# Performance work log

Measured on AMD Instinct MI355X. Metric: run time of the kernel, lower is better.

Reference implementation:

```python
import jax, jax.numpy as jnp
import numpy as np

INPUT_DIM = 10
SIG_DEPTH = 3
HIDDEN = 64
D_AUG = INPUT_DIM + 1  # time augmentation
LOGSIG_DIM = min(sum(D_AUG ** k // max(1, k) for k in range(1, SIG_DEPTH + 1)), 512)  # = 512
B, N = 1024, 256


def _compute_logsigs(features):
    """Vectorized computation of the per-step prefix-path signature features.

    For prefix length k+1 the torch code time-augments with linspace(0,1,k+1),
    i.e. dt = 1/k, which makes the time-related signature terms k-dependent.
    All terms reduce to cumulative sums over t, computed once for all k.
    Returns (B, N, LOGSIG_DIM); row k=0 is zeros (torch uses zeros at k=0).
    """
    Bsz, n, D = features.shape
    d = D + 1  # augmented dim (time first)
    dtype = features.dtype
    x0 = features[:, :1, :]
    inc = features[:, 1:, :] - features[:, :-1, :]          # (B, n-1, D) feature increments
    rel = features - x0                                      # x_t - x_0, (B, n, D)
    t_idx = jnp.arange(n - 1, dtype=dtype)
    # A[k-1] = sum_{t<k} t * dx_t   (time-row of level-2 term, before dt scaling)
    A = jnp.cumsum(t_idx[None, :, None] * inc, axis=1)       # (B, n-1, D)
    # Bc[k-1] = sum_{t=0}^{k-1} (x_t - x_0)   (time-column, before dt scaling)
    Bc = jnp.cumsum(rel[:, :-1, :], axis=1)                  # (B, n-1, D)
    # C[k-1] = sum_{t<k} (x_t - x_0) outer dx_t  (feature-feature level-2 block)
    C = jnp.cumsum(rel[:, :-1, :, None] * inc[:, :, None, :], axis=1)  # (B, n-1, D, D)
    ks = jnp.arange(1, n, dtype=dtype)                       # k = 1..n-1
    inv_k = 1.0 / ks
    tt = 0.5 * (ks - 1) * inv_k                              # sum t*dt^2 = (k-1)/(2k)
    # level-1: [T=1, x_k - x_0]
    sig1 = jnp.concatenate([jnp.ones((Bsz, n - 1, 1), dtype), rel[:, 1:, :]], axis=-1)  # (B, n-1, d)
    # level-2 matrix, augmented order [time, features]
    sig2 = jnp.zeros((Bsz, n - 1, d, d), dtype)
    sig2 = sig2.at[:, :, 0, 0].set(tt[None, :])
    sig2 = sig2.at[:, :, 0, 1:].set(inv_k[None, :, None] * A)
    sig2 = sig2.at[:, :, 1:, 0].set(inv_k[None, :, None] * Bc)
    sig2 = sig2.at[:, :, 1:, 1:].set(C)
    sig2f = sig2.reshape(Bsz, n - 1, d * d)
    # level-3 (torch: flatten(sig1 outer sig2_flat), truncated); only build needed rows
    sig3_len = LOGSIG_DIM - d - d * d                        # 512 - 11 - 121 = 380
    rows = (sig3_len + d * d - 1) // (d * d)                 # 4 rows of sig1 suffice
    sig3 = (sig1[..., :rows, None] * sig2f[..., None, :]).reshape(Bsz, n - 1, rows * d * d)[..., :sig3_len]
    logsig = jnp.concatenate([sig1, sig2f, sig3], axis=-1)[..., :LOGSIG_DIM]  # (B, n-1, 512)
    return jnp.concatenate([jnp.zeros((Bsz, 1, LOGSIG_DIM), dtype), logsig], axis=1)


def setup_inputs() -> dict:
    key = jax.random.key(0)
    k0, k1, k2, k3 = jax.random.split(key, 4)
    features = jax.random.normal(k0, (B, N, INPUT_DIM), jnp.float32)
    in_dim = LOGSIG_DIM + INPUT_DIM + 1  # 523
    W1 = jax.random.normal(k1, (in_dim, HIDDEN), jnp.float32) / np.sqrt(in_dim)
    b1 = jnp.zeros((HIDDEN,), jnp.float32)
    W2 = jax.random.normal(k2, (HIDDEN, HIDDEN), jnp.float32) / np.sqrt(HIDDEN)
    b2 = jnp.zeros((HIDDEN,), jnp.float32)
    W3 = jax.random.normal(k3, (HIDDEN, 1), jnp.float32) / np.sqrt(HIDDEN)
    b3 = jnp.zeros((1,), jnp.float32)
    return {"features": features, "W1": W1, "b1": b1, "W2": W2, "b2": b2, "W3": W3, "b3": b3}


def reference(features, W1, b1, W2, b2, W3, b3):
    logsigs = _compute_logsigs(features)  # (B, N, LOGSIG_DIM)
    Bsz = features.shape[0]

    def step(prev_delta, inputs):
        ls, ft = inputs  # (B, L), (B, D)
        x = jnp.concatenate([ls, ft, prev_delta], axis=-1)
        h = jax.nn.relu(x @ W1 + b1)
        h = jax.nn.relu(h @ W2 + b2)
        delta = h @ W3 + b3  # (B, 1)
        return delta, delta[:, 0]

    ls_t = jnp.swapaxes(logsigs, 0, 1)   # (N, B, L)
    ft_t = jnp.swapaxes(features, 0, 1)  # (N, B, D)
    _, deltas = jax.lax.scan(step, jnp.zeros((Bsz, 1), features.dtype), (ls_t, ft_t))
    return jnp.swapaxes(deltas, 0, 1)    # (B, N)
```

## Files before the change

### kernel.cpp

```cpp
#include <hip/hip_runtime.h>

#define NB 1024
#define NT 256
#define IND 10
#define HID 64

#define KSTEPS 14
#define XS 456
#define WMF_HALVES (KSTEPS * 4 * 64 * 8)

typedef short bf16x8 __attribute__((ext_vector_type(8)));
typedef float f32x4 __attribute__((ext_vector_type(4)));

__device__ __forceinline__ int qmap(int kk) {
    if (kk < 10) return 1 + kk;
    if (kk < 20) return 11 * (kk - 10 + 1);
    int i = (kk - 20) / 10, c = (kk - 20) % 10;
    return 11 * (i + 1) + 1 + c;
}

__device__ __forceinline__ unsigned bf16rne(float x) {
    unsigned u = __float_as_uint(x);
    return (u + 0x7fffu + ((u >> 16) & 1u)) >> 16;
}
__device__ __forceinline__ unsigned pk2(float a, float b) {
    return bf16rne(a) | (bf16rne(b) << 16);
}

__device__ float wm_value(int kk, int j, const float* __restrict__ W1,
                          const float* __restrict__ b1) {
    if (kk < 384) {
        int sec = kk >> 7;
        int rem = kk & 127;
        int w = rem >> 5, i = rem & 31;
        if (i >= 30) return 0.f;
        int q = qmap(30 * w + i);
        if (sec == 0) return W1[(11 + q) * 64 + j] + W1[(132 + q) * 64 + j];
        if (sec == 1) return W1[(253 + q) * 64 + j];
        return W1[(374 + q) * 64 + j];
    }
    if (kk < 400) {
        int i = kk - 384;
        if (i < 10) return W1[(496 + i) * 64 + j];
        if (i == 10) return W1[506 * 64 + j];
        return W1[(507 + (i - 11)) * 64 + j];
    }
    if (kk < 410) return W1[(1 + (kk - 400)) * 64 + j];
    if (kk < 420) return W1[(512 + (kk - 410)) * 64 + j];
    if (kk == 420) return W1[11 * 64 + j] + W1[132 * 64 + j];
    if (kk == 421) return W1[253 * 64 + j];
    if (kk == 422) return W1[374 * 64 + j];
    if (kk == 423) return W1[495 * 64 + j];
    if (kk == 424) return W1[0 * 64 + j];
    if (kk == 425) return b1[j];
    return 0.f;
}

__global__ void pack_mfma_kernel(const float* __restrict__ W1,
                                 const float* __restrict__ b1,
                                 unsigned short* __restrict__ Wmf) {
    int idx = blockIdx.x * 256 + threadIdx.x;
    if (idx >= WMF_HALVES) return;
    int half = idx & 7;
    int lane = (idx >> 3) & 63;
    int rec = idx >> 9;
    int s = rec >> 2, jb = rec & 3;
    int kk = 32 * s + (lane >> 4) * 8 + half;
    int j = 16 * jb + (lane & 15);
    Wmf[idx] = (unsigned short)bf16rne(wm_value(kk, j, W1, b1));
}

__global__ __launch_bounds__(256, 1) void presig9_kernel(
    const float* __restrict__ features, const unsigned short* __restrict__ Wmf,
    float* __restrict__ pre1) {
    const int b = blockIdx.x;
    const int tid = threadIdx.x;
    const int l = tid & 63;
    const int wu = tid >> 6;

    __shared__ __align__(16) float sF[NT * IND];
    __shared__ __align__(16) unsigned short sX[64 * XS];
    __shared__ float sBase[128];

    {
        const float4* src = (const float4*)(features + b * (NT * IND));
        float4* dst = (float4*)sF;
        for (int e = tid; e < NT * IND / 4; e += 256) dst[e] = src[e];
    }
    float f0[IND];
#pragma unroll
    for (int c = 0; c < IND; ++c) f0[c] = features[b * (NT * IND) + c];

    if (tid < 128) sBase[tid] = 0.f;
    __syncthreads();

    for (int tile = 0; tile < 4; ++tile) {
        const int t0 = tile * 64;

        const int r = t0 + l;
        float rf = (float)r;
        float fr[IND], rel[IND], inc[IND];
#pragma unroll
        for (int c = 0; c < IND; ++c) fr[c] = sF[r * IND + c];
#pragma unroll
        for (int c = 0; c < IND; ++c) rel[c] = fr[c] - f0[c];
        {
            bool last = (r >= NT - 1);
#pragma unroll
            for (int c = 0; c < IND; ++c)
                inc[c] = last ? 0.f : (sF[(r + 1) * IND + c] - fr[c]);
        }
        float p[30], own[30];
        if (wu == 0) {
#pragma unroll
            for (int c = 0; c < 10; ++c) p[c] = rf * inc[c];
#pragma unroll
            for (int i = 0; i < 10; ++i) p[10 + i] = rel[i];
#pragma unroll
            for (int c = 0; c < 10; ++c) p[20 + c] = rel[0] * inc[c];
        } else {
            const int i0 = 3 * wu - 2;
#pragma unroll
            for (int q = 0; q < 30; ++q) {
                int i = i0 + q / 10, c = q % 10;
                p[q] = rel[i] * inc[c];
            }
        }
#pragma unroll
        for (int i = 0; i < 30; ++i) own[i] = p[i];
#pragma unroll
        for (int dsh = 0; dsh < 6; ++dsh) {
            const int d = 1 << dsh;
            bool ok = (l >= d);
#pragma unroll
            for (int i = 0; i < 30; ++i) {
                float v = __shfl_up(p[i], d, 64);
                if (ok) p[i] += v;
            }
        }
        float inv_r = (r > 0) ? 1.f / rf : 0.f;
        float v[30];
#pragma unroll
        for (int i = 0; i < 30; ++i) {
            float x = sBase[wu * 32 + i] + p[i] - own[i];
            if (wu == 0 && i < 20) x *= inv_r;
            v[i] = x;
        }

        {
            float g0 = rel[0], g1 = rel[1];
            uint4* xr = (uint4*)&sX[l * XS];
            uint4* x0 = (uint4*)&sX[l * XS + 128];
            uint4* x1 = (uint4*)&sX[l * XS + 256];
            int qb = 8 * wu;
#pragma unroll
            for (int q = 0; q < 3; ++q) {
                uint4 tr, t0v, t1v;
                tr.x = pk2(v[8*q+0], v[8*q+1]); tr.y = pk2(v[8*q+2], v[8*q+3]);
                tr.z = pk2(v[8*q+4], v[8*q+5]); tr.w = pk2(v[8*q+6], v[8*q+7]);
                t0v.x = pk2(g0*v[8*q+0], g0*v[8*q+1]); t0v.y = pk2(g0*v[8*q+2], g0*v[8*q+3]);
                t0v.z = pk2(g0*v[8*q+4], g0*v[8*q+5]); t0v.w = pk2(g0*v[8*q+6], g0*v[8*q+7]);
                t1v.x = pk2(g1*v[8*q+0], g1*v[8*q+1]); t1v.y = pk2(g1*v[8*q+2], g1*v[8*q+3]);
                t1v.z = pk2(g1*v[8*q+4], g1*v[8*q+5]); t1v.w = pk2(g1*v[8*q+6], g1*v[8*q+7]);
                xr[wu * 4 + q] = tr; x0[wu * 4 + q] = t0v; x1[wu * 4 + q] = t1v;
            }
            {
                uint4 tr, t0v, t1v;
                tr.x = pk2(v[24], v[25]); tr.y = pk2(v[26], v[27]);
                tr.z = pk2(v[28], v[29]); tr.w = 0u;
                t0v.x = pk2(g0*v[24], g0*v[25]); t0v.y = pk2(g0*v[26], g0*v[27]);
                t0v.z = pk2(g0*v[28], g0*v[29]); t0v.w = 0u;
                t1v.x = pk2(g1*v[24], g1*v[25]); t1v.y = pk2(g1*v[26], g1*v[27]);
                t1v.z = pk2(g1*v[28], g1*v[29]); t1v.w = 0u;
                xr[wu * 4 + 3] = tr; x0[wu * 4 + 3] = t0v; x1[wu * 4 + 3] = t1v;
            }
            (void)qb;
        }
        if (wu == 0) {
            float g2 = rel[2];
            float ttv = 0.5f * (rf - 1.f) * inv_r;
            float gate = (r > 0) ? 1.f : 0.f;
            uint4* xe = (uint4*)&sX[l * XS + 384];
            uint4 u;
            u.x = pk2(g2*v[0], g2*v[1]);  u.y = pk2(g2*v[2], g2*v[3]);
            u.z = pk2(g2*v[4], g2*v[5]);  u.w = pk2(g2*v[6], g2*v[7]);
            xe[0] = u;
            u.x = pk2(g2*v[8], g2*v[9]);  u.y = pk2(g2*v[10], g2*v[20]);
            u.z = pk2(g2*v[21], g2*v[22]); u.w = pk2(g2*v[23], g2*v[24]);
            xe[1] = u;
            u.x = pk2(rel[0], rel[1]); u.y = pk2(rel[2], rel[3]);
            u.z = pk2(rel[4], rel[5]); u.w = pk2(rel[6], rel[7]);
            xe[2] = u;
            u.x = pk2(rel[8], rel[9]); u.y = pk2(fr[0], fr[1]);
            u.z = pk2(fr[2], fr[3]);   u.w = pk2(fr[4], fr[5]);
            xe[3] = u;
            u.x = pk2(fr[6], fr[7]); u.y = pk2(fr[8], fr[9]);
            u.z = pk2(ttv, ttv * rel[0]); u.w = pk2(ttv * rel[1], ttv * rel[2]);
            xe[4] = u;
            u.x = pk2(gate, 1.0f); u.y = 0u; u.z = 0u; u.w = 0u;
            xe[5] = u;
            u.x = 0u; u.y = 0u; u.z = 0u; u.w = 0u;
            xe[6] = u; xe[7] = u;
        }
        if (l == 63) {
#pragma unroll
            for (int i = 0; i < 30; ++i) sBase[wu * 32 + i] += p[i];
        }
        __syncthreads();

        {
            const int m = l & 15, quad = l >> 4;
            const unsigned short* arow = &sX[(16 * wu + m) * XS + 8 * quad];
            const bf16x8* bp = (const bf16x8*)Wmf;
            f32x4 ac0 = {0.f, 0.f, 0.f, 0.f}, ac1 = ac0, ac2 = ac0, ac3 = ac0;
#pragma unroll
            for (int s = 0; s < KSTEPS; ++s) {
                bf16x8 af = *(const bf16x8*)(arow + 32 * s);
                bf16x8 bf0 = bp[(s * 4 + 0) * 64 + l];
                bf16x8 bf1 = bp[(s * 4 + 1) * 64 + l];
                bf16x8 bf2 = bp[(s * 4 + 2) * 64 + l];
                bf16x8 bf3 = bp[(s * 4 + 3) * 64 + l];
                ac0 = __builtin_amdgcn_mfma_f32_16x16x32_bf16(af, bf0, ac0, 0, 0, 0);
                ac1 = __builtin_amdgcn_mfma_f32_16x16x32_bf16(af, bf1, ac1, 0, 0, 0);
                ac2 = __builtin_amdgcn_mfma_f32_16x16x32_bf16(af, bf2, ac2, 0, 0, 0);
                ac3 = __builtin_amdgcn_mfma_f32_16x16x32_bf16(af, bf3, ac3, 0, 0, 0);
            }
            float* op = pre1 + b * (NT * HID) + (t0 + 16 * wu) * HID + m;
            const int rowb = quad * 4;
#pragma unroll
            for (int reg = 0; reg < 4; ++reg) {
                op[(rowb + reg) * HID + 0]  = ac0[reg];
                op[(rowb + reg) * HID + 16] = ac1[reg];
                op[(rowb + reg) * HID + 32] = ac2[reg];
                op[(rowb + reg) * HID + 48] = ac3[reg];
            }
        }
        __syncthreads();
    }
}

template <int CTRL, int RMASK>
__device__ __forceinline__ float dpp_add(float x) {
    int v = __builtin_amdgcn_update_dpp(0, __float_as_int(x), CTRL, RMASK, 0xf, false);
    return x + __int_as_float(v);
}

#define W2_EACH(X) X(0) X(1) X(2) X(3) X(4) X(5) X(6) X(7) \
    X(8) X(9) X(10) X(11) X(12) X(13) X(14) X(15)

__global__ __launch_bounds__(64, 1) void scan_kernel(
    const float* __restrict__ pre1, const float* __restrict__ W1,
    const float* __restrict__ W2, const float* __restrict__ b2,
    const float* __restrict__ W3, const float* __restrict__ b3,
    float* __restrict__ out) {
    const int b = blockIdx.x;
    const int j = threadIdx.x;

    __shared__ __align__(16) float sH[64];

#define DECLW(q) float4 w2_##q = make_float4( \
        W2[(4*(q)+0)*64 + j], W2[(4*(q)+1)*64 + j], \
        W2[(4*(q)+2)*64 + j], W2[(4*(q)+3)*64 + j]);
    W2_EACH(DECLW)
#undef DECLW
    float w1l = W1[522 * 64 + j];
    float b2j = b2[j], w3j = W3[j], b3v = b3[0];

    const float* pb_ = pre1 + b * (NT * HID);
    float delta = 0.f;
    float outbuf = 0.f;

#define GEMVQ(q) { float4 h4 = *(const float4*)&sH[4*(q)]; \
        a0 = fmaf(h4.x, w2_##q.x, a0); a1 = fmaf(h4.y, w2_##q.y, a1); \
        a2 = fmaf(h4.z, w2_##q.z, a2); a3 = fmaf(h4.w, w2_##q.w, a3); }

#define SCAN_STEP(pv, mm) { \
        float h1 = fmaxf(fmaf(delta, w1l, (pv)), 0.f); \
        sH[j] = h1; \
        float a0 = 0.f, a1 = 0.f, a2 = 0.f, a3 = 0.f; \
        W2_EACH(GEMVQ) \
        float h2 = fmaxf((a0 + a1) + (a2 + a3) + b2j, 0.f); \
        float qv = h2 * w3j; \
        qv = dpp_add<0x111, 0xf>(qv); \
        qv = dpp_add<0x112, 0xf>(qv); \
        qv = dpp_add<0x114, 0xf>(qv); \
        qv = dpp_add<0x118, 0xf>(qv); \
        qv = dpp_add<0x142, 0xa>(qv); \
        qv = dpp_add<0x143, 0xc>(qv); \
        float tot = __uint_as_float(__builtin_amdgcn_readlane(__float_as_uint(qv), 63)); \
        delta = tot + b3v; \
        if (j == ((mm) & 63)) outbuf = delta; \
        if (((mm) & 63) == 63) out[b * NT + ((mm) & ~63) + j] = outbuf; }

    float r0 = pb_[0 * 64 + j], r1 = pb_[1 * 64 + j], r2 = pb_[2 * 64 + j],
          r3 = pb_[3 * 64 + j], r4 = pb_[4 * 64 + j], r5 = pb_[5 * 64 + j],
          r6 = pb_[6 * 64 + j], r7 = pb_[7 * 64 + j];
    for (int g = 0; g < NT; g += 8) {
        int nb = g + 8;
        float n0 = pb_[min(nb + 0, NT - 1) * 64 + j];
        float n1 = pb_[min(nb + 1, NT - 1) * 64 + j];
        float n2 = pb_[min(nb + 2, NT - 1) * 64 + j];
        float n3 = pb_[min(nb + 3, NT - 1) * 64 + j];
        float n4 = pb_[min(nb + 4, NT - 1) * 64 + j];
        float n5 = pb_[min(nb + 5, NT - 1) * 64 + j];
        float n6 = pb_[min(nb + 6, NT - 1) * 64 + j];
        float n7 = pb_[min(nb + 7, NT - 1) * 64 + j];
        SCAN_STEP(r0, g + 0)
        SCAN_STEP(r1, g + 1)
        SCAN_STEP(r2, g + 2)
        SCAN_STEP(r3, g + 3)
        SCAN_STEP(r4, g + 4)
        SCAN_STEP(r5, g + 5)
        SCAN_STEP(r6, g + 6)
        SCAN_STEP(r7, g + 7)
        r0 = n0; r1 = n1; r2 = n2; r3 = n3; r4 = n4; r5 = n5; r6 = n6; r7 = n7;
    }
#undef SCAN_STEP
#undef GEMVQ
}

__global__ __launch_bounds__(256) void logsig_hedge_fallback(
    const float* __restrict__ features, const float* __restrict__ W1,
    const float* __restrict__ b1, const float* __restrict__ W2,
    const float* __restrict__ b2, const float* __restrict__ W3,
    const float* __restrict__ b3, float* __restrict__ out) {
    const int b = blockIdx.x;
    const int tid = threadIdx.x;
    const int j = tid & 63;
    const int s = tid >> 6;

    __shared__ __align__(16) float sF[NT * IND];
    __shared__ __align__(16) float sSig[128];
    __shared__ float sA[IND], sB[IND], sC[IND * IND];
    __shared__ float sRel[IND];
    __shared__ __align__(16) float sPart[4 * 64];
    __shared__ __align__(16) float sH1[64];

    for (int idx = tid; idx < NT * IND; idx += 256)
        sF[idx] = features[b * (NT * IND) + idx];
    if (tid < 100) sC[tid] = 0.f;
    else if (tid < 110) sA[tid - 100] = 0.f;
    else if (tid < 120) sB[tid - 110] = 0.f;
    else if (tid >= 121 && tid < 128) sSig[tid] = 0.f;

    float vs[32], vb[32], vc[32];
#pragma unroll
    for (int mm = 0; mm < 32; ++mm) {
        int mp = 32 * s + mm;
        if (mp < 121) {
            vs[mm] = W1[(11 + mp) * 64 + j] + W1[(132 + mp) * 64 + j];
            vb[mm] = W1[(253 + mp) * 64 + j];
            vc[mm] = W1[(374 + mp) * 64 + j];
        } else { vs[mm] = 0.f; vb[mm] = 0.f; vc[mm] = 0.f; }
    }
    float ex[17];
#pragma unroll
    for (int q = 0; q < 17; ++q) ex[q] = 0.f;
    if (s == 1) {
#pragma unroll
        for (int q = 0; q < 11; ++q) ex[q] = W1[q * 64 + j];
    } else if (s == 2) {
#pragma unroll
        for (int q = 0; q < 10; ++q) ex[q] = W1[(512 + q) * 64 + j];
        ex[10] = b1[j];
    } else if (s == 3) {
#pragma unroll
        for (int q = 0; q < 17; ++q) ex[q] = W1[(495 + q) * 64 + j];
    }
    float w2p[16];
#pragma unroll
    for (int ii = 0; ii < 16; ++ii) w2p[ii] = W2[(16 * s + ii) * 64 + j];

    float w1l = 0.f, b2j = 0.f, w3j = 0.f, b3v = 0.f;
    if (s == 0) { w1l = W1[522 * 64 + j]; b2j = b2[j]; w3j = W3[j]; b3v = b3[0]; }
    float delta = 0.f;

    __syncthreads();

    for (int m = 0; m < NT; ++m) {
        if (m > 0) {
            if (tid < 100) {
                int i = tid / 10, c = tid % 10;
                float rp = sF[(m - 1) * 10 + i] - sF[i];
                float ic = sF[m * 10 + c] - sF[(m - 1) * 10 + c];
                sC[tid] += rp * ic;
            } else if (tid < 110) {
                int i = tid - 100;
                sA[i] += (float)(m - 1) * (sF[m * 10 + i] - sF[(m - 1) * 10 + i]);
            } else if (tid < 120) {
                int i = tid - 110;
                sB[i] += sF[(m - 1) * 10 + i] - sF[i];
            }
            __syncthreads();
            float inv_k = 1.0f / (float)m;
            if (tid == 0) sSig[0] = 0.5f * (float)(m - 1) * inv_k;
            else if (tid < 11) sSig[tid] = inv_k * sA[tid - 1];
            else if (tid < 121) {
                int i = tid / 11 - 1, c = tid % 11;
                sSig[tid] = (c == 0) ? inv_k * sB[i] : sC[i * 10 + (c - 1)];
            } else if (tid < 131) {
                int f = tid - 121;
                sRel[f] = sF[m * 10 + f] - sF[f];
            }
            __syncthreads();
        }
        float part = 0.f;
        if (m > 0) {
            float pa = 0.f, pb = 0.f, pc = 0.f;
#pragma unroll
            for (int q = 0; q < 8; ++q) {
                float4 sv = *(const float4*)&sSig[32 * s + 4 * q];
                pa = fmaf(sv.x, vs[4 * q + 0], pa);
                pb = fmaf(sv.x, vb[4 * q + 0], pb);
                pc = fmaf(sv.x, vc[4 * q + 0], pc);
                pa = fmaf(sv.y, vs[4 * q + 1], pa);
                pb = fmaf(sv.y, vb[4 * q + 1], pb);
                pc = fmaf(sv.y, vc[4 * q + 1], pc);
                pa = fmaf(sv.z, vs[4 * q + 2], pa);
                pb = fmaf(sv.z, vb[4 * q + 2], pb);
                pc = fmaf(sv.z, vc[4 * q + 2], pc);
                pa = fmaf(sv.w, vs[4 * q + 3], pa);
                pb = fmaf(sv.w, vb[4 * q + 3], pb);
                pc = fmaf(sv.w, vc[4 * q + 3], pc);
            }
            part = pa + sRel[0] * pb + sRel[1] * pc;
            if (s == 3) {
                float pd = 0.f;
#pragma unroll
                for (int q = 0; q < 17; ++q) pd = fmaf(sSig[q], ex[q], pd);
                part = fmaf(sRel[2], pd, part);
            }
            if (s == 1) {
                part += ex[0];
#pragma unroll
                for (int i = 0; i < 10; ++i) part = fmaf(sRel[i], ex[1 + i], part);
            }
        }
        if (s == 2) {
            float pf = ex[10];
#pragma unroll
            for (int f = 0; f < 10; ++f) pf = fmaf(sF[m * 10 + f], ex[f], pf);
            part += pf;
        }
        sPart[s * 64 + j] = part;
        __syncthreads();
        if (s == 0) {
            float x = sPart[j] + sPart[64 + j] + sPart[128 + j] + sPart[192 + j];
            sH1[j] = fmaxf(fmaf(delta, w1l, x), 0.f);
        }
        __syncthreads();
        {
            float hp = 0.f;
#pragma unroll
            for (int q = 0; q < 4; ++q) {
                float4 hv = *(const float4*)&sH1[16 * s + 4 * q];
                hp = fmaf(hv.x, w2p[4 * q + 0], hp);
                hp = fmaf(hv.y, w2p[4 * q + 1], hp);
                hp = fmaf(hv.z, w2p[4 * q + 2], hp);
                hp = fmaf(hv.w, w2p[4 * q + 3], hp);
            }
            sPart[s * 64 + j] = hp;
        }
        __syncthreads();
        if (s == 0) {
            float x2 = sPart[j] + sPart[64 + j] + sPart[128 + j] + sPart[192 + j] + b2j;
            float h2 = fmaxf(x2, 0.f);
            float dv = h2 * w3j;
#pragma unroll
            for (int off = 32; off > 0; off >>= 1) dv += __shfl_xor(dv, off, 64);
            delta = dv + b3v;
            if (j == 0) out[b * NT + m] = delta;
        }
        __syncthreads();
    }
}

extern "C" void kernel_launch(void* const* d_in, const int* in_sizes, int n_in,
                              void* d_out, int out_size, void* d_ws, size_t ws_size,
                              hipStream_t stream) {
    const float* features = (const float*)d_in[0];
    const float* W1 = (const float*)d_in[1];
    const float* b1 = (const float*)d_in[2];
    const float* W2 = (const float*)d_in[3];
    const float* b2 = (const float*)d_in[4];
    const float* W3 = (const float*)d_in[5];
    const float* b3 = (const float*)d_in[6];
    float* out = (float*)d_out;

    const size_t wmf_bytes = (size_t)WMF_HALVES * 2;
    const size_t w_pad     = ((wmf_bytes + 255) / 256) * 256;
    const size_t pre_bytes = (size_t)NB * NT * HID * sizeof(float);
    if (ws_size >= w_pad + pre_bytes) {
        unsigned short* Wmf = (unsigned short*)d_ws;
        float* pre1 = (float*)((char*)d_ws + w_pad);
        pack_mfma_kernel<<<(WMF_HALVES + 255) / 256, 256, 0, stream>>>(W1, b1, Wmf);
        presig9_kernel<<<NB, 256, 0, stream>>>(features, Wmf, pre1);
        scan_kernel<<<NB, 64, 0, stream>>>(pre1, W1, W2, b2, W3, b3, out);
    } else {
        logsig_hedge_fallback<<<NB, 256, 0, stream>>>(features, W1, b1, W2, b2, W3, b3, out);
    }
}
```

Baseline: 282.6 us.

## Batch 16 paths per wave in scan and run W2 GEMV on bf16 MFMA

Replaces the per-path scan kernel (one 64-lane wave per batch row, scalar GEMV through LDS) with a kernel where each wave advances 16 batch rows together. The 64x64 hidden layer runs as bf16 16x16x32 MFMAs, with W2 held in registers as MFMA fragments. The output reduction uses row-level DPP adds, and each row's delta is broadcast back with shuffles. It adds a cheap round-to-bf16 packing helper based on perm. The aim is a shorter serial per-step latency chain with no LDS round trip, at the cost of bf16 precision on h1 and W2 and a grid of only 64 workgroups.

```diff
diff --git a/kernel.cpp b/kernel.cpp
--- a/kernel.cpp
+++ b/kernel.cpp
@@ -11,6 +11,7 @@
 
 typedef short bf16x8 __attribute__((ext_vector_type(8)));
 typedef float f32x4 __attribute__((ext_vector_type(4)));
+typedef unsigned u32x4 __attribute__((ext_vector_type(4)));
 
 __device__ __forceinline__ int qmap(int kk) {
     if (kk < 10) return 1 + kk;
@@ -25,6 +26,11 @@
 }
 __device__ __forceinline__ unsigned pk2(float a, float b) {
     return bf16rne(a) | (bf16rne(b) << 16);
+}
+__device__ __forceinline__ unsigned pk2f(float a, float b) {
+    unsigned ua = __float_as_uint(a) + 0x8000u;
+    unsigned ub = __float_as_uint(b) + 0x8000u;
+    return __builtin_amdgcn_perm(ub, ua, 0x07060302u);
 }
 
 __device__ float wm_value(int kk, int j, const float* __restrict__ W1,
@@ -152,7 +158,6 @@
             uint4* xr = (uint4*)&sX[l * XS];
             uint4* x0 = (uint4*)&sX[l * XS + 128];
             uint4* x1 = (uint4*)&sX[l * XS + 256];
-            int qb = 8 * wu;
 #pragma unroll
             for (int q = 0; q < 3; ++q) {
                 uint4 tr, t0v, t1v;
@@ -174,7 +179,6 @@
                 t1v.z = pk2(g1*v[28], g1*v[29]); t1v.w = 0u;
                 xr[wu * 4 + 3] = tr; x0[wu * 4 + 3] = t0v; x1[wu * 4 + 3] = t1v;
             }
-            (void)qb;
         }
         if (wu == 0) {
             float g2 = rel[2];
@@ -245,78 +249,147 @@
     return x + __int_as_float(v);
 }
 
-#define W2_EACH(X) X(0) X(1) X(2) X(3) X(4) X(5) X(6) X(7) \
-    X(8) X(9) X(10) X(11) X(12) X(13) X(14) X(15)
-
-__global__ __launch_bounds__(64, 1) void scan_kernel(
+__global__ __launch_bounds__(64, 1) void scan5_kernel(
     const float* __restrict__ pre1, const float* __restrict__ W1,
     const float* __restrict__ W2, const float* __restrict__ b2,
     const float* __restrict__ W3, const float* __restrict__ b3,
     float* __restrict__ out) {
-    const int b = blockIdx.x;
-    const int j = threadIdx.x;
-
-    __shared__ __align__(16) float sH[64];
-
-#define DECLW(q) float4 w2_##q = make_float4( \
-        W2[(4*(q)+0)*64 + j], W2[(4*(q)+1)*64 + j], \
-        W2[(4*(q)+2)*64 + j], W2[(4*(q)+3)*64 + j]);
-    W2_EACH(DECLW)
-#undef DECLW
-    float w1l = W1[522 * 64 + j];
-    float b2j = b2[j], w3j = W3[j], b3v = b3[0];
-
-    const float* pb_ = pre1 + b * (NT * HID);
+    const int l = threadIdx.x;
+    const int m = l & 15;
+    const int quad = l >> 4;
+    const int b0 = blockIdx.x * 16;
+
+    float w1a[8], w1b[8];
+#pragma unroll
+    for (int ii = 0; ii < 8; ++ii) {
+        w1a[ii] = W1[522 * 64 + quad * 8 + ii];
+        w1b[ii] = W1[522 * 64 + 32 + quad * 8 + ii];
+    }
+    bf16x8 wf[4][2];
+#pragma unroll
+    for (int nb = 0; nb < 4; ++nb)
+#pragma unroll
+        for (int kh = 0; kh < 2; ++kh) {
+            u32x4 u;
+#pragma unroll
+            for (int q = 0; q < 4; ++q) {
+                int k0 = kh * 32 + quad * 8 + 2 * q;
+                u[q] = pk2(W2[k0 * 64 + nb * 16 + m], W2[(k0 + 1) * 64 + nb * 16 + m]);
+            }
+            wf[nb][kh] = __builtin_bit_cast(bf16x8, u);
+        }
+    float b2v[4], w3v[4];
+#pragma unroll
+    for (int nb = 0; nb < 4; ++nb) { b2v[nb] = b2[nb * 16 + m]; w3v[nb] = W3[nb * 16 + m]; }
+    float b3v = b3[0];
+
+    const float* base = pre1 + (size_t)(b0 + m) * (NT * HID) + quad * 8;
     float delta = 0.f;
-    float outbuf = 0.f;
-
-#define GEMVQ(q) { float4 h4 = *(const float4*)&sH[4*(q)]; \
-        a0 = fmaf(h4.x, w2_##q.x, a0); a1 = fmaf(h4.y, w2_##q.y, a1); \
-        a2 = fmaf(h4.z, w2_##q.z, a2); a3 = fmaf(h4.w, w2_##q.w, a3); }
-
-#define SCAN_STEP(pv, mm) { \
-        float h1 = fmaxf(fmaf(delta, w1l, (pv)), 0.f); \
-        sH[j] = h1; \
-        float a0 = 0.f, a1 = 0.f, a2 = 0.f, a3 = 0.f; \
-        W2_EACH(GEMVQ) \
-        float h2 = fmaxf((a0 + a1) + (a2 + a3) + b2j, 0.f); \
-        float qv = h2 * w3j; \
-        qv = dpp_add<0x111, 0xf>(qv); \
-        qv = dpp_add<0x112, 0xf>(qv); \
-        qv = dpp_add<0x114, 0xf>(qv); \
-        qv = dpp_add<0x118, 0xf>(qv); \
-        qv = dpp_add<0x142, 0xa>(qv); \
-        qv = dpp_add<0x143, 0xc>(qv); \
-        float tot = __uint_as_float(__builtin_amdgcn_readlane(__float_as_uint(qv), 63)); \
-        delta = tot + b3v; \
-        if (j == ((mm) & 63)) outbuf = delta; \
-        if (((mm) & 63) == 63) out[b * NT + ((mm) & ~63) + j] = outbuf; }
-
-    float r0 = pb_[0 * 64 + j], r1 = pb_[1 * 64 + j], r2 = pb_[2 * 64 + j],
-          r3 = pb_[3 * 64 + j], r4 = pb_[4 * 64 + j], r5 = pb_[5 * 64 + j],
-          r6 = pb_[6 * 64 + j], r7 = pb_[7 * 64 + j];
-    for (int g = 0; g < NT; g += 8) {
-        int nb = g + 8;
-        float n0 = pb_[min(nb + 0, NT - 1) * 64 + j];
-        float n1 = pb_[min(nb + 1, NT - 1) * 64 + j];
-        float n2 = pb_[min(nb + 2, NT - 1) * 64 + j];
-        float n3 = pb_[min(nb + 3, NT - 1) * 64 + j];
-        float n4 = pb_[min(nb + 4, NT - 1) * 64 + j];
-        float n5 = pb_[min(nb + 5, NT - 1) * 64 + j];
-        float n6 = pb_[min(nb + 6, NT - 1) * 64 + j];
-        float n7 = pb_[min(nb + 7, NT - 1) * 64 + j];
-        SCAN_STEP(r0, g + 0)
-        SCAN_STEP(r1, g + 1)
-        SCAN_STEP(r2, g + 2)
-        SCAN_STEP(r3, g + 3)
-        SCAN_STEP(r4, g + 4)
-        SCAN_STEP(r5, g + 5)
-        SCAN_STEP(r6, g + 6)
-        SCAN_STEP(r7, g + 7)
-        r0 = n0; r1 = n1; r2 = n2; r3 = n3; r4 = n4; r5 = n5; r6 = n6; r7 = n7;
-    }
-#undef SCAN_STEP
-#undef GEMVQ
+
+    float4 f00 = *(const float4*)(base + 0 * HID);
+    float4 f01 = *(const float4*)(base + 0 * HID + 4);
+    float4 f02 = *(const float4*)(base + 0 * HID + 32);
+    float4 f03 = *(const float4*)(base + 0 * HID + 36);
+    float4 f10 = *(const float4*)(base + 1 * HID);
+    float4 f11 = *(const float4*)(base + 1 * HID + 4);
+    float4 f12 = *(const float4*)(base + 1 * HID + 32);
+    float4 f13 = *(const float4*)(base + 1 * HID + 36);
+
+    for (int t = 0; t < NT; ++t) {
+        int tp = (t + 2 < NT) ? (t + 2) : (NT - 1);
+        float4 g0 = *(const float4*)(base + tp * HID);
+        float4 g1 = *(const float4*)(base + tp * HID + 4);
+        float4 g2 = *(const float4*)(base + tp * HID + 32);
+        float4 g3 = *(const float4*)(base + tp * HID + 36);
+
+        u32x4 ua, ub;
+        {
+            float h0 = fmaxf(fmaf(delta, w1a[0], f00.x), 0.f);
+            float h1 = fmaxf(fmaf(delta, w1a[1], f00.y), 0.f);
+            float h2 = fmaxf(fmaf(delta, w1a[2], f00.z), 0.f);
+            float h3 = fmaxf(fmaf(delta, w1a[3], f00.w), 0.f);
+            float h4 = fmaxf(fmaf(delta, w1a[4], f01.x), 0.f);
+            float h5 = fmaxf(fmaf(delta, w1a[5], f01.y), 0.f);
+            float h6 = fmaxf(fmaf(delta, w1a[6], f01.z), 0.f);
+            float h7 = fmaxf(fmaf(delta, w1a[7], f01.w), 0.f);
+            ua[0] = pk2f(h0, h1); ua[1] = pk2f(h2, h3);
+            ua[2] = pk2f(h4, h5); ua[3] = pk2f(h6, h7);
+            float k0 = fmaxf(fmaf(delta, w1b[0], f02.x), 0.f);
+            float k1 = fmaxf(fmaf(delta, w1b[1], f02.y), 0.f);
+            float k2 = fmaxf(fmaf(delta, w1b[2], f02.z), 0.f);
+            float k3 = fmaxf(fmaf(delta, w1b[3], f02.w), 0.f);
+            float k4 = fmaxf(fmaf(delta, w1b[4], f03.x), 0.f);
+            float k5 = fmaxf(fmaf(delta, w1b[5], f03.y), 0.f);
+            float k6 = fmaxf(fmaf(delta, w1b[6], f03.z), 0.f);
+            float k7 = fmaxf(fmaf(delta, w1b[7], f03.w), 0.f);
+            ub[0] = pk2f(k0, k1); ub[1] = pk2f(k2, k3);
+            ub[2] = pk2f(k4, k5); ub[3] = pk2f(k6, k7);
+        }
+        bf16x8 af0 = __builtin_bit_cast(bf16x8, ua);
+        bf16x8 af1 = __builtin_bit_cast(bf16x8, ub);
+
+        f32x4 z = {0.f, 0.f, 0.f, 0.f};
+        f32x4 ac0 = __builtin_amdgcn_mfma_f32_16x16x32_bf16(af0, wf[0][0], z, 0, 0, 0);
+        f32x4 ac1 = __builtin_amdgcn_mfma_f32_16x16x32_bf16(af0, wf[1][0], z, 0, 0, 0);
+        f32x4 ac2 = __builtin_amdgcn_mfma_f32_16x16x32_bf16(af0, wf[2][0], z, 0, 0, 0);
+        f32x4 ac3 = __builtin_amdgcn_mfma_f32_16x16x32_bf16(af0, wf[3][0], z, 0, 0, 0);
+        ac0 = __builtin_amdgcn_mfma_f32_16x16x32_bf16(af1, wf[0][1], ac0, 0, 0, 0);
+        ac1 = __builtin_amdgcn_mfma_f32_16x16x32_bf16(af1, wf[1][1], ac1, 0, 0, 0);
+        ac2 = __builtin_amdgcn_mfma_f32_16x16x32_bf16(af1, wf[2][1], ac2, 0, 0, 0);
+        ac3 = __builtin_amdgcn_mfma_f32_16x16x32_bf16(af1, wf[3][1], ac3, 0, 0, 0);
+
+        float s0, s1, s2, s3;
+        {
+            float q00 = fmaxf(ac0[0] + b2v[0], 0.f) * w3v[0];
+            float q01 = fmaxf(ac1[0] + b2v[1], 0.f) * w3v[1];
+            float q02 = fmaxf(ac2[0] + b2v[2], 0.f) * w3v[2];
+            float q03 = fmaxf(ac3[0] + b2v[3], 0.f) * w3v[3];
+            s0 = (q00 + q01) + (q02 + q03);
+            float q10 = fmaxf(ac0[1] + b2v[0], 0.f) * w3v[0];
+            float q11 = fmaxf(ac1[1] + b2v[1], 0.f) * w3v[1];
+            float q12 = fmaxf(ac2[1] + b2v[2], 0.f) * w3v[2];
+            float q13 = fmaxf(ac3[1] + b2v[3], 0.f) * w3v[3];
+            s1 = (q10 + q11) + (q12 + q13);
+            float q20 = fmaxf(ac0[2] + b2v[0], 0.f) * w3v[0];
+            float q21 = fmaxf(ac1[2] + b2v[1], 0.f) * w3v[1];
+            float q22 = fmaxf(ac2[2] + b2v[2], 0.f) * w3v[2];
+            float q23 = fmaxf(ac3[2] + b2v[3], 0.f) * w3v[3];
+            s2 = (q20 + q21) + (q22 + q23);
+            float q30 = fmaxf(ac0[3] + b2v[0], 0.f) * w3v[0];
+            float q31 = fmaxf(ac1[3] + b2v[1], 0.f) * w3v[1];
+            float q32 = fmaxf(ac2[3] + b2v[2], 0.f) * w3v[2];
+            float q33 = fmaxf(ac3[3] + b2v[3], 0.f) * w3v[3];
+            s3 = (q30 + q31) + (q32 + q33);
+        }
+        s0 = dpp_add<0x128, 0xf>(s0); s1 = dpp_add<0x128, 0xf>(s1);
+        s2 = dpp_add<0x128, 0xf>(s2); s3 = dpp_add<0x128, 0xf>(s3);
+        s0 = dpp_add<0x124, 0xf>(s0); s1 = dpp_add<0x124, 0xf>(s1);
+        s2 = dpp_add<0x124, 0xf>(s2); s3 = dpp_add<0x124, 0xf>(s3);
+        s0 = dpp_add<0x122, 0xf>(s0); s1 = dpp_add<0x122, 0xf>(s1);
+        s2 = dpp_add<0x122, 0xf>(s2); s3 = dpp_add<0x122, 0xf>(s3);
+        s0 = dpp_add<0x121, 0xf>(s0); s1 = dpp_add<0x121, 0xf>(s1);
+        s2 = dpp_add<0x121, 0xf>(s2); s3 = dpp_add<0x121, 0xf>(s3);
+        s0 += b3v; s1 += b3v; s2 += b3v; s3 += b3v;
+
+        if (m == 0) {
+            out[(b0 + quad * 4 + 0) * NT + t] = s0;
+            out[(b0 + quad * 4 + 1) * NT + t] = s1;
+            out[(b0 + quad * 4 + 2) * NT + t] = s2;
+            out[(b0 + quad * 4 + 3) * NT + t] = s3;
+        }
+        {
+            int src = (m >> 2) << 4;
+            float d0 = __shfl(s0, src, 64);
+            float d1 = __shfl(s1, src, 64);
+            float d2 = __shfl(s2, src, 64);
+            float d3 = __shfl(s3, src, 64);
+            float t01 = (m & 1) ? d1 : d0;
+            float t23 = (m & 1) ? d3 : d2;
+            delta = (m & 2) ? t23 : t01;
+        }
+        f00 = f10; f01 = f11; f02 = f12; f03 = f13;
+        f10 = g0; f11 = g1; f12 = g2; f13 = g3;
+    }
 }
 
 __global__ __launch_bounds__(256) void logsig_hedge_fallback(
@@ -495,7 +568,7 @@
         float* pre1 = (float*)((char*)d_ws + w_pad);
         pack_mfma_kernel<<<(WMF_HALVES + 255) / 256, 256, 0, stream>>>(W1, b1, Wmf);
         presig9_kernel<<<NB, 256, 0, stream>>>(features, Wmf, pre1);
-        scan_kernel<<<NB, 64, 0, stream>>>(pre1, W1, W2, b2, W3, b3, out);
+        scan5_kernel<<<64, 64, 0, stream>>>(pre1, W1, W2, b2, W3, b3, out);
     } else {
         logsig_hedge_fallback<<<NB, 256, 0, stream>>>(features, W1, b1, W2, b2, W3, b3, out);
     }
```

Measured after the change: 309.5 us. 1.1x slower.
